# Kernel tuning notes

Hardware: AMD Instinct MI355X
Metric: run time of the kernel (lower is better)

The kernel has to match this reference:

```python
import jax, jax.numpy as jnp
import numpy as np

B, S, E, H = 4, 2048, 1024, 16
D = E // H


def setup_inputs() -> dict:
    key = jax.random.key(0)
    ks = jax.random.split(key, 4)
    scale = 0.02
    x = jax.random.normal(ks[0], (B, S, E), dtype=jnp.float32)
    in_proj_w = jax.random.normal(ks[1], (3 * E, E), dtype=jnp.float32) * scale
    in_proj_b = jnp.zeros((3 * E,), dtype=jnp.float32)
    out_w = jax.random.normal(ks[2], (E, E), dtype=jnp.float32) * scale
    out_b = jnp.zeros((E,), dtype=jnp.float32)
    rel_bias = jax.random.normal(ks[3], (2 * 32 + 1, H), dtype=jnp.float32) * 0.02
    return {"x": x, "in_proj_w": in_proj_w, "in_proj_b": in_proj_b,
            "out_w": out_w, "out_b": out_b, "rel_bias": rel_bias,
            "max_rel_dist": 32}


def reference(x, in_proj_w, in_proj_b, out_w, out_b, rel_bias, max_rel_dist):
    b, s, e = x.shape
    h = rel_bias.shape[1]
    d = e // h
    # relative-position indices, clamped: [S, S]
    i = jnp.arange(s)[:, None]
    j = jnp.arange(s)[None, :]
    rel = jnp.clip(i - j, -max_rel_dist, max_rel_dist) + max_rel_dist
    # gather per-pair per-head bias then average over heads -> single 2D mask
    attn_mask = jnp.mean(rel_bias[rel], axis=-1)  # [S, S]
    # fused QKV projection (PyTorch in_proj: x @ W^T + b)
    qkv = x @ in_proj_w.T + in_proj_b           # [B, S, 3E]
    q, k, v = jnp.split(qkv, 3, axis=-1)
    q = q.reshape(b, s, h, d)
    k = k.reshape(b, s, h, d)
    v = v.reshape(b, s, h, d)
    scale = 1.0 / jnp.sqrt(jnp.asarray(d, dtype=x.dtype))
    scores = jnp.einsum('bqhd,bkhd->bhqk', q, k) * scale + attn_mask  # [B,H,S,S]
    probs = jax.nn.softmax(scores, axis=-1)
    ctx = jnp.einsum('bhqk,bkhd->bqhd', probs, v).reshape(b, s, e)
    return ctx @ out_w.T + out_b
```

## Files before the change

kernel.cpp:

```cpp
#include <hip/hip_runtime.h>
#include <math.h>

#define B_ 4
#define S_ 2048
#define E_ 1024
#define H_ 16
#define D_ 64
#define MRD 32

typedef __bf16 bf16x8 __attribute__((ext_vector_type(8)));
typedef float f32x4 __attribute__((ext_vector_type(4)));
typedef unsigned short us8 __attribute__((ext_vector_type(8)));
typedef unsigned short us4 __attribute__((ext_vector_type(4)));

union frag_cvt { us8 u; bf16x8 b; };
union h_cvt { __bf16 h; unsigned short u; };

__device__ __forceinline__ unsigned short bhi(float x) {
    h_cvt c; c.h = (__bf16)x; return c.u;
}
__device__ __forceinline__ float bf16_f(unsigned short h) {
    union { unsigned int u; float f; } c;
    c.u = ((unsigned int)h) << 16;
    return c.f;
}

__device__ __forceinline__ void async_copy16(const void* g, void* l) {
    __builtin_amdgcn_global_load_lds(
        (const __attribute__((address_space(1))) void*)g,
        (__attribute__((address_space(3))) void*)l,
        16, 0, 0);
}

__device__ __forceinline__ f32x4 mf16(const frag_cvt& a, const frag_cvt& b, f32x4 c) {
    return __builtin_amdgcn_mfma_f32_16x16x32_bf16(a.b, b.b, c, 0, 0, 0);
}

#define QSCL 0.18033688f
#define L2E  1.44269504f

__global__ __launch_bounds__(128) void cvt_bf16(
    const float* __restrict__ in, unsigned short* __restrict__ out, int K)
{
    const int r  = blockIdx.x;
    const int k8 = threadIdx.x * 8;
    if (k8 >= K) return;
    const float* p = in + (size_t)r * K + k8;
    float4 a = *(const float4*)p;
    float4 b = *(const float4*)(p + 4);
    float xs[8] = {a.x, a.y, a.z, a.w, b.x, b.y, b.z, b.w};
    us8 hu;
#pragma unroll
    for (int j = 0; j < 8; ++j) hu[j] = bhi(xs[j]);
    *(us8*)&out[(size_t)r * K + k8] = hu;
}

__global__ __launch_bounds__(128) void split_hilo(
    const float* __restrict__ in, unsigned short* __restrict__ out, int K)
{
    const int r  = blockIdx.x;
    const int k8 = threadIdx.x * 8;
    if (k8 >= K) return;
    const float* p = in + (size_t)r * K + k8;
    float4 a = *(const float4*)p;
    float4 b = *(const float4*)(p + 4);
    float xs[8] = {a.x, a.y, a.z, a.w, b.x, b.y, b.z, b.w};
    us8 hu, lu;
#pragma unroll
    for (int j = 0; j < 8; ++j) {
        unsigned short hb = bhi(xs[j]);
        hu[j] = hb;
        lu[j] = bhi(xs[j] - bf16_f(hb));
    }
    *(us8*)&out[(size_t)r * 2 * K + k8]     = hu;
    *(us8*)&out[(size_t)r * 2 * K + K + k8] = lu;
}

__device__ __forceinline__ void stage_unit(const unsigned short* g, int grs,
                                           unsigned short* lu, int t)
{
#pragma unroll
    for (int l = 0; l < 2; ++l) {
        const int f  = l * 512 + t;
        const int ri = f >> 3;
        const int cs = ((f & 7) ^ (ri & 7)) * 8;
        async_copy16(g + (size_t)ri * grs + cs,
                     lu + l * 4096 + (t >> 6) * 512);
    }
}

template<int MODE>
__global__ __launch_bounds__(512, 2) void gemm8(
    const unsigned short* __restrict__ Ag, const unsigned short* __restrict__ Bg,
    const float* __restrict__ bias,
    unsigned short* __restrict__ O0, unsigned short* __restrict__ O1,
    unsigned short* __restrict__ O2, float* __restrict__ Cf)
{
    constexpr int KD = (MODE == 0) ? 1024 : 3072;
    constexpr int NT = KD / 64;
    constexpr int AS = (MODE == 0) ? 1024 : 2048;
    constexpr int BS = (MODE == 0) ? 1024 : 2048;

    __shared__ unsigned short sbuf[2][24576];

    const int t    = threadIdx.x;
    const int lane = t & 63;
    const int w    = t >> 6;
    const int ln   = lane & 15;
    const int quad = lane >> 4;
    const int wm   = w >> 1;
    const int wn   = w & 1;
    const int m0   = blockIdx.x * 256;
    const int n0   = blockIdx.y * 128;

    auto mapA = [](int kk) -> int {
        return (MODE == 0) ? kk : (kk < 1024 ? kk : kk - 1024);
    };
    auto mapB = [](int kk) -> int {
        return (MODE == 0) ? kk : (kk < 2048 ? kk : kk - 2048);
    };

    const int swz = (ln & 7) << 3;
    const int kq0 = (quad * 8) ^ swz;
    const int kq1 = (32 + quad * 8) ^ swz;

    f32x4 acc[4][4];
#pragma unroll
    for (int i = 0; i < 4; ++i)
#pragma unroll
        for (int j = 0; j < 4; ++j)
            acc[i][j] = (f32x4){0.f, 0.f, 0.f, 0.f};

    stage_unit(Ag + (size_t)m0 * AS + mapA(0),          AS, &sbuf[0][0],     t);
    stage_unit(Ag + (size_t)(m0 + 128) * AS + mapA(0),  AS, &sbuf[0][8192],  t);
    stage_unit(Bg + (size_t)n0 * BS + mapB(0),          BS, &sbuf[0][16384], t);
    stage_unit(Ag + (size_t)m0 * AS + mapA(64),         AS, &sbuf[1][0],     t);
    stage_unit(Ag + (size_t)(m0 + 128) * AS + mapA(64), AS, &sbuf[1][8192],  t);
    stage_unit(Bg + (size_t)n0 * BS + mapB(64),         BS, &sbuf[1][16384], t);
    asm volatile("s_waitcnt vmcnt(6)" ::: "memory");
    __builtin_amdgcn_s_barrier();

    for (int k = 0; k < NT; ++k) {
        unsigned short* bufc = sbuf[k & 1];
        frag_cvt af[4][2], bg[4][2];

#pragma unroll
        for (int i = 0; i < 4; ++i) {
            const int ra = (wm * 64 + i * 16 + ln) * 64;
            af[i][0].u = *(const us8*)&bufc[ra + kq0];
            af[i][1].u = *(const us8*)&bufc[ra + kq1];
            const int rb = 16384 + (wn * 64 + i * 16 + ln) * 64;
            bg[i][0].u = *(const us8*)&bufc[rb + kq0];
            bg[i][1].u = *(const us8*)&bufc[rb + kq1];
        }
        __builtin_amdgcn_s_setprio(1);
#pragma unroll
        for (int i = 0; i < 4; ++i)
#pragma unroll
            for (int j = 0; j < 4; ++j) {
                acc[i][j] = mf16(af[i][0], bg[j][0], acc[i][j]);
                acc[i][j] = mf16(af[i][1], bg[j][1], acc[i][j]);
            }
        __builtin_amdgcn_s_setprio(0);

        if (k == NT - 1) break;

        __builtin_amdgcn_s_barrier();

        if (k + 2 < NT) {
            const int kk = (k + 2) * 64;
            stage_unit(Ag + (size_t)m0 * AS + mapA(kk),         AS, &bufc[0],     t);
            stage_unit(Ag + (size_t)(m0 + 128) * AS + mapA(kk), AS, &bufc[8192],  t);
            stage_unit(Bg + (size_t)n0 * BS + mapB(kk),         BS, &bufc[16384], t);
            asm volatile("s_waitcnt vmcnt(6)" ::: "memory");
        } else {
            asm volatile("s_waitcnt vmcnt(0)" ::: "memory");
        }

        __builtin_amdgcn_s_barrier();
    }

    if constexpr (MODE == 0) {
        if (n0 < E_) {
#pragma unroll
            for (int j = 0; j < 4; ++j) {
                const int col = n0 + wn * 64 + j * 16 + ln;
                const float bv = bias[col];
                const int h = (col & (E_ - 1)) >> 6, d = col & 63;
#pragma unroll
                for (int i = 0; i < 4; ++i) {
#pragma unroll
                    for (int r = 0; r < 4; ++r) {
                        const int row = m0 + wm * 64 + i * 16 + quad * 4 + r;
                        const int b = row >> 11, s = row & (S_ - 1);
                        O0[((size_t)(b * 16 + h) * S_ + s) * 64 + d] =
                            bhi((acc[i][j][r] + bv) * QSCL);
                    }
                }
            }
        } else if (n0 < 2 * E_) {
#pragma unroll
            for (int j = 0; j < 4; ++j) {
                const int col = n0 + wn * 64 + j * 16 + ln;
                const float bv = bias[col];
                const int h = (col & (E_ - 1)) >> 6, d = col & 63;
#pragma unroll
                for (int i = 0; i < 4; ++i) {
#pragma unroll
                    for (int r = 0; r < 4; ++r) {
                        const int row = m0 + wm * 64 + i * 16 + quad * 4 + r;
                        const int b = row >> 11, s = row & (S_ - 1);
                        O1[((size_t)(b * 16 + h) * S_ + s) * 64 +
                           (((d >> 3) ^ (s & 7)) * 8) + (d & 7)] =
                            bhi(acc[i][j][r] + bv);
                    }
                }
            }
        } else {
#pragma unroll
            for (int j = 0; j < 4; ++j) {
                const int col = n0 + wn * 64 + j * 16 + ln;
                const float bv = bias[col];
                const int h = (col & (E_ - 1)) >> 6, d = col & 63;
#pragma unroll
                for (int i = 0; i < 4; ++i) {
                    const int row0 = m0 + wm * 64 + i * 16 + quad * 4;
                    const int b = row0 >> 11, s0 = row0 & (S_ - 1);
                    const int tile = s0 >> 6;
                    const int g = (s0 >> 3) & 7;
                    us4 o;
#pragma unroll
                    for (int r = 0; r < 4; ++r) o[r] = bhi(acc[i][j][r] + bv);
                    *(us4*)&O2[(size_t)(b * 16 + h) * S_ * 64 + tile * 4096 +
                               d * 64 + ((g ^ (d & 7)) * 8) + (quad & 1) * 4] = o;
                }
            }
        }
    } else {
#pragma unroll
        for (int j = 0; j < 4; ++j) {
            const int col = n0 + wn * 64 + j * 16 + ln;
            const float bv = bias[col];
#pragma unroll
            for (int i = 0; i < 4; ++i) {
                const int row = m0 + wm * 64 + i * 16 + quad * 4;
#pragma unroll
                for (int r = 0; r < 4; ++r)
                    Cf[(size_t)(row + r) * E_ + col] = acc[i][j][r] + bv;
            }
        }
    }
}

__global__ __launch_bounds__(256, 4) void attn_mfma5(
    const unsigned short* __restrict__ Qb, const unsigned short* __restrict__ K2,
    const unsigned short* __restrict__ Vt2, const float* __restrict__ rel_bias,
    unsigned short* __restrict__ ctx2)
{
    __shared__ unsigned short Kt[64 * 64];
    __shared__ unsigned short Vt[64 * 64];
    __shared__ unsigned short Pt[128 * 72];
    __shared__ float bias_s[65];

    const int t    = threadIdx.x;
    const int w    = t >> 6;
    const int lane = t & 63;
    const int ln   = lane & 15;
    const int quad = lane >> 4;

    const int bh = blockIdx.x;
    const int b  = bh >> 4;
    const int h  = bh & 15;
    const int q0 = blockIdx.y * 128;

    if (t < 65) {
        float s = 0.f;
#pragma unroll
        for (int hh = 0; hh < 16; ++hh) s += rel_bias[t * 16 + hh];
        bias_s[t] = s * (L2E / 16.f);
    }

    frag_cvt qf[2][2];
#pragma unroll
    for (int mf = 0; mf < 2; ++mf) {
        const unsigned short* qp =
            Qb + ((size_t)bh * S_ + q0 + w * 32 + mf * 16 + ln) * 64;
        qf[mf][0].u = *(const us8*)(qp + quad * 8);
        qf[mf][1].u = *(const us8*)(qp + 32 + quad * 8);
    }

    frag_cvt ones;
#pragma unroll
    for (int j = 0; j < 8; ++j) ones.u[j] = 0x3F80;

    f32x4 O[2][4];
#pragma unroll
    for (int mf = 0; mf < 2; ++mf)
#pragma unroll
        for (int n = 0; n < 4; ++n) O[mf][n] = (f32x4){0.f, 0.f, 0.f, 0.f};
    f32x4 lacc[2] = {(f32x4){0.f, 0.f, 0.f, 0.f}, (f32x4){0.f, 0.f, 0.f, 0.f}};

    const unsigned short* Kg = K2  + (size_t)bh * S_ * 64;
    const unsigned short* Vg = Vt2 + (size_t)bh * S_ * 64;

    for (int k0 = 0; k0 < S_; k0 += 64) {
        __syncthreads();
        {
            const unsigned short* kg = Kg + (size_t)k0 * 64;
            const unsigned short* vg = Vg + (size_t)k0 * 64;
            const int uo = w * 512;
            async_copy16(kg + uo + lane * 8,        &Kt[uo]);
            async_copy16(kg + 2048 + uo + lane * 8, &Kt[2048 + uo]);
            async_copy16(vg + uo + lane * 8,        &Vt[uo]);
            async_copy16(vg + 2048 + uo + lane * 8, &Vt[2048 + uo]);
        }
        __syncthreads();

        f32x4 sa[2][4];
#pragma unroll
        for (int n = 0; n < 4; ++n) {
            sa[0][n] = (f32x4){0.f, 0.f, 0.f, 0.f};
            sa[1][n] = (f32x4){0.f, 0.f, 0.f, 0.f};
            const int ro = (n * 16 + ln) * 64;
#pragma unroll
            for (int ks = 0; ks < 2; ++ks) {
                frag_cvt kh;
                kh.u = *(const us8*)&Kt[ro + (((ks * 4 + quad) ^ (ln & 7)) * 8)];
                sa[0][n] = __builtin_amdgcn_mfma_f32_16x16x32_bf16(
                    qf[0][ks].b, kh.b, sa[0][n], 0, 0, 0);
                sa[1][n] = __builtin_amdgcn_mfma_f32_16x16x32_bf16(
                    qf[1][ks].b, kh.b, sa[1][n], 0, 0, 0);
            }
        }

        const bool inband = (k0 >= q0 - 64) && (k0 <= q0 + 128);
        float cb = 0.f;
        if (!inband) cb = bias_s[(k0 < q0) ? 64 : 0];
#pragma unroll
        for (int mf = 0; mf < 2; ++mf) {
#pragma unroll
            for (int n = 0; n < 4; ++n) {
#pragma unroll
                for (int r = 0; r < 4; ++r) {
                    float s2;
                    if (inband) {
                        const int q   = q0 + w * 32 + mf * 16 + quad * 4 + r;
                        const int key = k0 + n * 16 + ln;
                        int rel = q - key;
                        rel = (rel < -MRD) ? -MRD : (rel > MRD ? MRD : rel);
                        s2 = sa[mf][n][r] + bias_s[rel + MRD];
                    } else {
                        s2 = sa[mf][n][r] + cb;
                    }
                    const int qrow = w * 32 + mf * 16 + quad * 4 + r;
                    const int pos = (n * 16 + ln) ^ ((qrow & 8) << 1);
                    Pt[qrow * 72 + pos] = bhi(__builtin_amdgcn_exp2f(s2));
                }
            }
        }

#pragma unroll
        for (int ks = 0; ks < 2; ++ks) {
            frag_cvt pa[2];
#pragma unroll
            for (int mf = 0; mf < 2; ++mf) {
                const int prow = w * 32 + mf * 16 + ln;
                pa[mf].u = *(const us8*)&Pt[prow * 72 +
                           ((ks * 32 + quad * 8) ^ ((prow & 8) << 1))];
                lacc[mf] = __builtin_amdgcn_mfma_f32_16x16x32_bf16(
                    pa[mf].b, ones.b, lacc[mf], 0, 0, 0);
            }
#pragma unroll
            for (int n = 0; n < 4; ++n) {
                frag_cvt vh;
                vh.u = *(const us8*)&Vt[(n * 16 + ln) * 64 +
                                        (((ks * 4 + quad) ^ (ln & 7)) * 8)];
                O[0][n] = __builtin_amdgcn_mfma_f32_16x16x32_bf16(
                    pa[0].b, vh.b, O[0][n], 0, 0, 0);
                O[1][n] = __builtin_amdgcn_mfma_f32_16x16x32_bf16(
                    pa[1].b, vh.b, O[1][n], 0, 0, 0);
            }
        }
    }

#pragma unroll
    for (int mf = 0; mf < 2; ++mf) {
        float inv[4];
#pragma unroll
        for (int r = 0; r < 4; ++r) inv[r] = 1.f / lacc[mf][r];
#pragma unroll
        for (int n = 0; n < 4; ++n) {
            const int k = h * D_ + n * 16 + ln;
#pragma unroll
            for (int r = 0; r < 4; ++r) {
                const int q = q0 + w * 32 + mf * 16 + quad * 4 + r;
                const float v = O[mf][n][r] * inv[r];
                unsigned short hb = bhi(v);
                const size_t rb = (size_t)(b * S_ + q) * (2 * E_);
                ctx2[rb + k]      = hb;
                ctx2[rb + E_ + k] = bhi(v - bf16_f(hb));
            }
        }
    }
}

extern "C" void kernel_launch(void* const* d_in, const int* in_sizes, int n_in,
                              void* d_out, int out_size, void* d_ws, size_t ws_size,
                              hipStream_t stream)
{
    const float* x         = (const float*)d_in[0];
    const float* in_proj_w = (const float*)d_in[1];
    const float* in_proj_b = (const float*)d_in[2];
    const float* out_w     = (const float*)d_in[3];
    const float* out_b     = (const float*)d_in[4];
    const float* rel_bias  = (const float*)d_in[5];
    float* out = (float*)d_out;

    const int M = B_ * S_;
    const size_t PH = (size_t)B_ * H_ * S_ * 64;

    unsigned short* Qb   = (unsigned short*)d_ws;
    unsigned short* K2   = Qb + PH;
    unsigned short* Vt2  = K2 + PH;
    unsigned short* W2o  = Vt2 + PH;
    unsigned short* Wqkv = W2o + (size_t)E_ * 2 * E_;
    unsigned short* A2c  = Wqkv + (size_t)3 * E_ * E_;
    unsigned short* Axb  = A2c;

    cvt_bf16<<<M,      128, 0, stream>>>(x,         Axb,  E_);
    cvt_bf16<<<3 * E_, 128, 0, stream>>>(in_proj_w, Wqkv, E_);

    {
        dim3 grid(M / 256, (3 * E_) / 128);
        gemm8<0><<<grid, 512, 0, stream>>>(Axb, Wqkv, in_proj_b,
                                           Qb, K2, Vt2, nullptr);
    }
    {
        dim3 grid(B_ * H_, S_ / 128);
        attn_mfma5<<<grid, 256, 0, stream>>>(Qb, K2, Vt2, rel_bias, A2c);
    }
    split_hilo<<<E_, 128, 0, stream>>>(out_w, W2o, E_);
    {
        dim3 grid(M / 256, E_ / 128);
        gemm8<1><<<grid, 512, 0, stream>>>(A2c, W2o, out_b,
                                           nullptr, nullptr, nullptr, out);
    }
}
```

Measured before the change: 326.0 us.

## Enlarge GEMM tiles to 256x256 with 8-phase interleaved prefetch schedule

Both projection GEMMs now use 256x256 output tiles per 512-thread block instead of 256x128, and each wave computes a 128x64 sub-tile. The K loop is restructured into four MFMA phases that interleave LDS fragment loads, next-tile global prefetch into the other buffer, and barriers, replacing the previous two-stage-ahead prefetch. The larger tile raises arithmetic intensity and reuse of staged data, at the cost of 128KB of shared memory, more accumulator registers per thread, and only one tile of prefetch depth, which may limit occupancy and latency hiding.

```diff
diff --git a/kernel.cpp b/kernel.cpp
--- a/kernel.cpp
+++ b/kernel.cpp
@@ -90,7 +90,7 @@
 }
 
 template<int MODE>
-__global__ __launch_bounds__(512, 2) void gemm8(
+__global__ __launch_bounds__(512, 2) void gemm256(
     const unsigned short* __restrict__ Ag, const unsigned short* __restrict__ Bg,
     const float* __restrict__ bias,
     unsigned short* __restrict__ O0, unsigned short* __restrict__ O1,
@@ -101,17 +101,17 @@
     constexpr int AS = (MODE == 0) ? 1024 : 2048;
     constexpr int BS = (MODE == 0) ? 1024 : 2048;
 
-    __shared__ unsigned short sbuf[2][24576];
+    __shared__ unsigned short sbuf[2][32768];
 
     const int t    = threadIdx.x;
     const int lane = t & 63;
     const int w    = t >> 6;
     const int ln   = lane & 15;
     const int quad = lane >> 4;
-    const int wm   = w >> 1;
-    const int wn   = w & 1;
+    const int wr   = w >> 2;
+    const int wc   = w & 3;
     const int m0   = blockIdx.x * 256;
-    const int n0   = blockIdx.y * 128;
+    const int n0   = blockIdx.y * 256;
 
     auto mapA = [](int kk) -> int {
         return (MODE == 0) ? kk : (kk < 1024 ? kk : kk - 1024);
@@ -124,9 +124,12 @@
     const int kq0 = (quad * 8) ^ swz;
     const int kq1 = (32 + quad * 8) ^ swz;
 
-    f32x4 acc[4][4];
-#pragma unroll
-    for (int i = 0; i < 4; ++i)
+    const int aBase = wr * 8192;
+    const int bBase = 16384 + (wc >> 1) * 8192 + (wc & 1) * 64 * 64;
+
+    f32x4 acc[8][4];
+#pragma unroll
+    for (int i = 0; i < 8; ++i)
 #pragma unroll
         for (int j = 0; j < 4; ++j)
             acc[i][j] = (f32x4){0.f, 0.f, 0.f, 0.f};
@@ -134,64 +137,112 @@
     stage_unit(Ag + (size_t)m0 * AS + mapA(0),          AS, &sbuf[0][0],     t);
     stage_unit(Ag + (size_t)(m0 + 128) * AS + mapA(0),  AS, &sbuf[0][8192],  t);
     stage_unit(Bg + (size_t)n0 * BS + mapB(0),          BS, &sbuf[0][16384], t);
-    stage_unit(Ag + (size_t)m0 * AS + mapA(64),         AS, &sbuf[1][0],     t);
-    stage_unit(Ag + (size_t)(m0 + 128) * AS + mapA(64), AS, &sbuf[1][8192],  t);
-    stage_unit(Bg + (size_t)n0 * BS + mapB(64),         BS, &sbuf[1][16384], t);
-    asm volatile("s_waitcnt vmcnt(6)" ::: "memory");
+    stage_unit(Bg + (size_t)(n0 + 128) * BS + mapB(0),  BS, &sbuf[0][24576], t);
+    asm volatile("s_waitcnt vmcnt(0)" ::: "memory");
     __builtin_amdgcn_s_barrier();
 
     for (int k = 0; k < NT; ++k) {
         unsigned short* bufc = sbuf[k & 1];
-        frag_cvt af[4][2], bg[4][2];
-
-#pragma unroll
-        for (int i = 0; i < 4; ++i) {
-            const int ra = (wm * 64 + i * 16 + ln) * 64;
-            af[i][0].u = *(const us8*)&bufc[ra + kq0];
-            af[i][1].u = *(const us8*)&bufc[ra + kq1];
-            const int rb = 16384 + (wn * 64 + i * 16 + ln) * 64;
-            bg[i][0].u = *(const us8*)&bufc[rb + kq0];
-            bg[i][1].u = *(const us8*)&bufc[rb + kq1];
-        }
+        unsigned short* bufn = sbuf[(k & 1) ^ 1];
+        const bool pf = (k + 1 < NT);
+        const int kk1 = (k + 1) * 64;
+        frag_cvt af0[4][2], af1[4][2], bf0[2][2], bf1[2][2];
+
+#pragma unroll
+        for (int ii = 0; ii < 4; ++ii) {
+            const int ra = aBase + (ii * 16 + ln) * 64;
+            af0[ii][0].u = *(const us8*)&bufc[ra + kq0];
+            af0[ii][1].u = *(const us8*)&bufc[ra + kq1];
+        }
+#pragma unroll
+        for (int j = 0; j < 2; ++j) {
+            const int rb = bBase + (j * 16 + ln) * 64;
+            bf0[j][0].u = *(const us8*)&bufc[rb + kq0];
+            bf0[j][1].u = *(const us8*)&bufc[rb + kq1];
+        }
+        if (pf) {
+            stage_unit(Ag + (size_t)m0 * AS + mapA(kk1),         AS, &bufn[0],    t);
+            stage_unit(Ag + (size_t)(m0 + 128) * AS + mapA(kk1), AS, &bufn[8192], t);
+        }
+        __builtin_amdgcn_s_barrier();
         __builtin_amdgcn_s_setprio(1);
 #pragma unroll
-        for (int i = 0; i < 4; ++i)
-#pragma unroll
-            for (int j = 0; j < 4; ++j) {
-                acc[i][j] = mf16(af[i][0], bg[j][0], acc[i][j]);
-                acc[i][j] = mf16(af[i][1], bg[j][1], acc[i][j]);
+        for (int ii = 0; ii < 4; ++ii)
+#pragma unroll
+            for (int j = 0; j < 2; ++j) {
+                acc[ii][j] = mf16(af0[ii][0], bf0[j][0], acc[ii][j]);
+                acc[ii][j] = mf16(af0[ii][1], bf0[j][1], acc[ii][j]);
             }
         __builtin_amdgcn_s_setprio(0);
-
-        if (k == NT - 1) break;
-
-        __builtin_amdgcn_s_barrier();
-
-        if (k + 2 < NT) {
-            const int kk = (k + 2) * 64;
-            stage_unit(Ag + (size_t)m0 * AS + mapA(kk),         AS, &bufc[0],     t);
-            stage_unit(Ag + (size_t)(m0 + 128) * AS + mapA(kk), AS, &bufc[8192],  t);
-            stage_unit(Bg + (size_t)n0 * BS + mapB(kk),         BS, &bufc[16384], t);
-            asm volatile("s_waitcnt vmcnt(6)" ::: "memory");
-        } else {
+        __builtin_amdgcn_s_barrier();
+
+#pragma unroll
+        for (int ii = 0; ii < 4; ++ii) {
+            const int ra = aBase + ((ii + 4) * 16 + ln) * 64;
+            af1[ii][0].u = *(const us8*)&bufc[ra + kq0];
+            af1[ii][1].u = *(const us8*)&bufc[ra + kq1];
+        }
+        if (pf) {
+            stage_unit(Bg + (size_t)n0 * BS + mapB(kk1),         BS, &bufn[16384], t);
+            stage_unit(Bg + (size_t)(n0 + 128) * BS + mapB(kk1), BS, &bufn[24576], t);
+        }
+        __builtin_amdgcn_s_barrier();
+        __builtin_amdgcn_s_setprio(1);
+#pragma unroll
+        for (int ii = 0; ii < 4; ++ii)
+#pragma unroll
+            for (int j = 0; j < 2; ++j) {
+                acc[ii + 4][j] = mf16(af1[ii][0], bf0[j][0], acc[ii + 4][j]);
+                acc[ii + 4][j] = mf16(af1[ii][1], bf0[j][1], acc[ii + 4][j]);
+            }
+        __builtin_amdgcn_s_setprio(0);
+        __builtin_amdgcn_s_barrier();
+
+#pragma unroll
+        for (int j = 0; j < 2; ++j) {
+            const int rb = bBase + ((j + 2) * 16 + ln) * 64;
+            bf1[j][0].u = *(const us8*)&bufc[rb + kq0];
+            bf1[j][1].u = *(const us8*)&bufc[rb + kq1];
+        }
+        __builtin_amdgcn_s_barrier();
+        __builtin_amdgcn_s_setprio(1);
+#pragma unroll
+        for (int ii = 0; ii < 4; ++ii)
+#pragma unroll
+            for (int j = 0; j < 2; ++j) {
+                acc[ii + 4][j + 2] = mf16(af1[ii][0], bf1[j][0], acc[ii + 4][j + 2]);
+                acc[ii + 4][j + 2] = mf16(af1[ii][1], bf1[j][1], acc[ii + 4][j + 2]);
+            }
+        __builtin_amdgcn_s_setprio(0);
+        __builtin_amdgcn_s_barrier();
+
+        __builtin_amdgcn_s_setprio(1);
+#pragma unroll
+        for (int ii = 0; ii < 4; ++ii)
+#pragma unroll
+            for (int j = 0; j < 2; ++j) {
+                acc[ii][j + 2] = mf16(af0[ii][0], bf1[j][0], acc[ii][j + 2]);
+                acc[ii][j + 2] = mf16(af0[ii][1], bf1[j][1], acc[ii][j + 2]);
+            }
+        __builtin_amdgcn_s_setprio(0);
+        if (pf) {
             asm volatile("s_waitcnt vmcnt(0)" ::: "memory");
-        }
-
-        __builtin_amdgcn_s_barrier();
+            __builtin_amdgcn_s_barrier();
+        }
     }
 
     if constexpr (MODE == 0) {
         if (n0 < E_) {
 #pragma unroll
             for (int j = 0; j < 4; ++j) {
-                const int col = n0 + wn * 64 + j * 16 + ln;
+                const int col = n0 + wc * 64 + j * 16 + ln;
                 const float bv = bias[col];
                 const int h = (col & (E_ - 1)) >> 6, d = col & 63;
 #pragma unroll
-                for (int i = 0; i < 4; ++i) {
+                for (int i = 0; i < 8; ++i) {
 #pragma unroll
                     for (int r = 0; r < 4; ++r) {
-                        const int row = m0 + wm * 64 + i * 16 + quad * 4 + r;
+                        const int row = m0 + wr * 128 + i * 16 + quad * 4 + r;
                         const int b = row >> 11, s = row & (S_ - 1);
                         O0[((size_t)(b * 16 + h) * S_ + s) * 64 + d] =
                             bhi((acc[i][j][r] + bv) * QSCL);
@@ -201,14 +252,14 @@
         } else if (n0 < 2 * E_) {
 #pragma unroll
             for (int j = 0; j < 4; ++j) {
-                const int col = n0 + wn * 64 + j * 16 + ln;
+                const int col = n0 + wc * 64 + j * 16 + ln;
                 const float bv = bias[col];
                 const int h = (col & (E_ - 1)) >> 6, d = col & 63;
 #pragma unroll
-                for (int i = 0; i < 4; ++i) {
+                for (int i = 0; i < 8; ++i) {
 #pragma unroll
                     for (int r = 0; r < 4; ++r) {
-                        const int row = m0 + wm * 64 + i * 16 + quad * 4 + r;
+                        const int row = m0 + wr * 128 + i * 16 + quad * 4 + r;
                         const int b = row >> 11, s = row & (S_ - 1);
                         O1[((size_t)(b * 16 + h) * S_ + s) * 64 +
                            (((d >> 3) ^ (s & 7)) * 8) + (d & 7)] =
@@ -219,12 +270,12 @@
         } else {
 #pragma unroll
             for (int j = 0; j < 4; ++j) {
-                const int col = n0 + wn * 64 + j * 16 + ln;
+                const int col = n0 + wc * 64 + j * 16 + ln;
                 const float bv = bias[col];
                 const int h = (col & (E_ - 1)) >> 6, d = col & 63;
 #pragma unroll
-                for (int i = 0; i < 4; ++i) {
-                    const int row0 = m0 + wm * 64 + i * 16 + quad * 4;
+                for (int i = 0; i < 8; ++i) {
+                    const int row0 = m0 + wr * 128 + i * 16 + quad * 4;
                     const int b = row0 >> 11, s0 = row0 & (S_ - 1);
                     const int tile = s0 >> 6;
                     const int g = (s0 >> 3) & 7;
@@ -239,11 +290,11 @@
     } else {
 #pragma unroll
         for (int j = 0; j < 4; ++j) {
-            const int col = n0 + wn * 64 + j * 16 + ln;
+            const int col = n0 + wc * 64 + j * 16 + ln;
             const float bv = bias[col];
 #pragma unroll
-            for (int i = 0; i < 4; ++i) {
-                const int row = m0 + wm * 64 + i * 16 + quad * 4;
+            for (int i = 0; i < 8; ++i) {
+                const int row = m0 + wr * 128 + i * 16 + quad * 4;
 #pragma unroll
                 for (int r = 0; r < 4; ++r)
                     Cf[(size_t)(row + r) * E_ + col] = acc[i][j][r] + bv;
@@ -431,9 +482,9 @@
     cvt_bf16<<<3 * E_, 128, 0, stream>>>(in_proj_w, Wqkv, E_);
 
     {
-        dim3 grid(M / 256, (3 * E_) / 128);
-        gemm8<0><<<grid, 512, 0, stream>>>(Axb, Wqkv, in_proj_b,
-                                           Qb, K2, Vt2, nullptr);
+        dim3 grid(M / 256, (3 * E_) / 256);
+        gemm256<0><<<grid, 512, 0, stream>>>(Axb, Wqkv, in_proj_b,
+                                             Qb, K2, Vt2, nullptr);
     }
     {
         dim3 grid(B_ * H_, S_ / 128);
@@ -441,8 +492,8 @@
     }
     split_hilo<<<E_, 128, 0, stream>>>(out_w, W2o, E_);
     {
-        dim3 grid(M / 256, E_ / 128);
-        gemm8<1><<<grid, 512, 0, stream>>>(A2c, W2o, out_b,
-                                           nullptr, nullptr, nullptr, out);
-    }
-}
+        dim3 grid(M / 256, E_ / 256);
+        gemm256<1><<<grid, 512, 0, stream>>>(A2c, W2o, out_b,
+                                             nullptr, nullptr, nullptr, out);
+    }
+}
```

After: 352.0 us. 1.08x slower.
